# Kernel tuning notes

Hardware: AMD Instinct MI355X
Metric: run time of the kernel (lower is better)

## Reference

```python
import jax, jax.numpy as jnp
import numpy as np

IMG = 512.0          # input H = W
SCORE_THR = 0.05
IOU_THR = 0.5
K_PRE = 1000         # pre-NMS candidates per image
MAX_DET = 300
CLS_OFF = 10000.0    # class-offset trick => per-class NMS


def _make_anchors():
    strides = [8, 16, 32, 64]
    sizes = [32.0, 64.0, 128.0, 256.0]
    ars = [0.5, 1.0, 2.0]
    out = []
    for s, sz in zip(strides, sizes):
        f = int(512 // s)
        ys, xs = np.meshgrid(np.arange(f), np.arange(f), indexing='ij')
        cx = (xs.reshape(-1) + 0.5) * s
        cy = (ys.reshape(-1) + 0.5) * s
        for ar in ars:
            w = sz * np.sqrt(ar)
            h = sz / np.sqrt(ar)
            out.append(np.stack([cx - w / 2, cy - h / 2, cx + w / 2, cy + h / 2], axis=1))
    return np.concatenate(out, axis=0).astype(np.float32)  # (16320, 4)


def setup_inputs() -> dict:
    key = jax.random.key(0)
    k1, k2 = jax.random.split(key)
    anchors = jnp.asarray(_make_anchors())
    B, C = 16, 80
    A = anchors.shape[0]
    cls_preds = jax.random.normal(k1, (B, A, C), jnp.float32) - 2.0  # logits, sigmoid ~0.12
    box_preds = jax.random.normal(k2, (B, A, 4), jnp.float32) * 0.2  # box deltas
    return {"cls_preds": cls_preds, "box_preds": box_preds, "anchors": anchors}


def _decode(anchors, deltas):
    aw = anchors[:, 2] - anchors[:, 0]
    ah = anchors[:, 3] - anchors[:, 1]
    acx = anchors[:, 0] + 0.5 * aw
    acy = anchors[:, 1] + 0.5 * ah
    cx = deltas[:, 0] * aw + acx
    cy = deltas[:, 1] * ah + acy
    w = jnp.exp(deltas[:, 2]) * aw
    h = jnp.exp(deltas[:, 3]) * ah
    b = jnp.stack([cx - 0.5 * w, cy - 0.5 * h, cx + 0.5 * w, cy + 0.5 * h], axis=1)
    return jnp.clip(b, 0.0, IMG)  # clamp to image, H == W == IMG


def _iou_matrix(b):
    area = jnp.maximum(b[:, 2] - b[:, 0], 0.0) * jnp.maximum(b[:, 3] - b[:, 1], 0.0)
    lt = jnp.maximum(b[:, None, :2], b[None, :, :2])
    rb = jnp.minimum(b[:, None, 2:], b[None, :, 2:])
    wh = jnp.clip(rb - lt, 0.0)
    inter = wh[..., 0] * wh[..., 1]
    return inter / jnp.maximum(area[:, None] + area[None, :] - inter, 1e-6)


def _per_image(cls_p, box_p, anchors):
    scores = jax.nn.sigmoid(cls_p)                 # (A, C)
    boxes = _decode(anchors, box_p)                # (A, 4)
    ms = scores.max(axis=1)                        # best class score
    lb = jnp.argmax(scores, axis=1)                # best class id (0-indexed)
    s = jnp.where(ms > SCORE_THR, ms, -1.0)        # score-threshold filter
    top_s, idx = jax.lax.top_k(s, K_PRE)           # pre-NMS candidates, sorted desc
    b = boxes[idx]
    l = lb[idx]
    ob = b + l[:, None].astype(b.dtype) * CLS_OFF  # per-class NMS via offset
    iou = _iou_matrix(ob)                          # (K_PRE, K_PRE)
    rng = jnp.arange(K_PRE)

    def body(i, keep):
        sup = (iou[i] > IOU_THR) & keep[i] & (rng > i)
        return keep & ~sup

    keep = jax.lax.fori_loop(0, K_PRE, body, top_s > 0.0)  # greedy NMS
    fs_all = jnp.where(keep, top_s, -1.0)
    fs, fi = jax.lax.top_k(fs_all, MAX_DET)
    ok = fs > 0.0
    out_boxes = jnp.where(ok[:, None], b[fi], 0.0)
    out_scores = jnp.where(ok, fs, 0.0)
    out_labels = jnp.where(ok, l[fi] + 1, 0)  # labels are 1-indexed
    return out_boxes, out_scores, out_labels


def reference(cls_preds, box_preds, anchors):
    return jax.vmap(lambda c, bp: _per_image(c, bp, anchors))(cls_preds, box_preds)
```

## Files before the change

kernel.cpp:

```cpp
#include <hip/hip_runtime.h>
#include <cstdint>
#include <cmath>

#define NB 16
#define AANCH 16320
#define NCLS 80
#define KPRE 1000
#define MAXDET 300
#define NCH 16
#define CANDCAP 16384
#define HBINS 8192

#define THR_LOGIT -2.9444389791664403f

__global__ __launch_bounds__(256) void k_score(const float* __restrict__ cls,
                                               uint32_t* __restrict__ key,
                                               int* __restrict__ label) {
    int b = blockIdx.y;
    int a0 = blockIdx.x * 64;
    int t = threadIdx.x;
    int al = t >> 2, g = t & 3;
    const float4* p = (const float4*)(cls + ((size_t)b * AANCH + a0) * NCLS) + al * 20 + g;
    float best = -3e38f; int bi = 0;
#pragma unroll
    for (int i = 0; i < 5; ++i) {
        float4 v = p[4 * i];
        int c0 = 4 * g + 16 * i;
        if (v.x > best) { best = v.x; bi = c0 + 0; }
        if (v.y > best) { best = v.y; bi = c0 + 1; }
        if (v.z > best) { best = v.z; bi = c0 + 2; }
        if (v.w > best) { best = v.w; bi = c0 + 3; }
    }
#pragma unroll
    for (int m = 1; m <= 2; m <<= 1) {
        float ob = __shfl_xor(best, m, 64);
        int oi = __shfl_xor(bi, m, 64);
        if (ob > best || (ob == best && oi < bi)) { best = ob; bi = oi; }
    }
    if (g == 0) {
        uint32_t k = 0;
        if (best > THR_LOGIT) {
            uint32_t ub = __float_as_uint(best);
            k = (ub & 0x80000000u) ? ~ub : (ub | 0x80000000u);
        }
        int ag = a0 + al;
        key[(size_t)b * AANCH + ag] = k;
        label[(size_t)b * AANCH + ag] = bi;
    }
}

__global__ __launch_bounds__(1024) void k_fsel(const uint32_t* __restrict__ key,
                                               uint32_t* __restrict__ validCount,
                                               uint32_t* __restrict__ candCount,
                                               uint32_t* __restrict__ candKey,
                                               uint32_t* __restrict__ candIdx) {
    __shared__ uint32_t kk[AANCH];
    __shared__ uint32_t hist[HBINS];
    __shared__ uint32_t part[256];
    __shared__ uint32_t s_pivot, s_pos;
    int b = blockIdx.x, tid = threadIdx.x;
    for (int i = tid; i < HBINS; i += 1024) hist[i] = 0;
    if (tid == 0) s_pos = 0;
    __syncthreads();
    const uint32_t* kb = key + (size_t)b * AANCH;
    for (int i = tid; i < AANCH; i += 1024) {
        uint32_t k = kb[i];
        kk[i] = k;
        atomicAdd(&hist[k >> 19], 1u);
    }
    __syncthreads();
    if (tid < 256) {
        uint32_t s = 0;
#pragma unroll
        for (int i = 0; i < 32; ++i) s += hist[tid * 32 + ((i + tid) & 31)];
        part[tid] = s;
    }
    __syncthreads();
    if (tid == 0) {
        uint32_t acc = 0; int tc = 0;
        for (int t2 = 255; t2 >= 0; --t2) {
            if (acc + part[t2] >= (uint32_t)KPRE) { tc = t2; break; }
            acc += part[t2];
        }
        uint32_t p1 = 0;
        for (int bin = tc * 32 + 31; bin >= tc * 32; --bin) {
            if (acc + hist[bin] >= (uint32_t)KPRE) { p1 = (uint32_t)bin; break; }
            acc += hist[bin];
        }
        s_pivot = p1;
        uint32_t nvalid = (uint32_t)AANCH - hist[0];
        validCount[b] = nvalid < (uint32_t)KPRE ? nvalid : (uint32_t)KPRE;
    }
    __syncthreads();
    uint32_t piv = s_pivot;
    for (int i = tid; i < AANCH; i += 1024) {
        uint32_t k = kk[i];
        if ((k >> 19) >= piv) {
            uint32_t pos = atomicAdd(&s_pos, 1u);
            if (pos < CANDCAP) {
                candKey[(size_t)b * CANDCAP + pos] = k;
                candIdx[(size_t)b * CANDCAP + pos] = (uint32_t)i;
            }
        }
    }
    __syncthreads();
    if (tid == 0) candCount[b] = s_pos < CANDCAP ? s_pos : CANDCAP;
}

__global__ __launch_bounds__(256) void k_rankdec(const uint32_t* __restrict__ candKey,
                                                 const uint32_t* __restrict__ candIdx,
                                                 const uint32_t* __restrict__ candCount,
                                                 const int* __restrict__ label,
                                                 const float* __restrict__ boxp,
                                                 const float* __restrict__ anchors,
                                                 float4* __restrict__ topBox,
                                                 float* __restrict__ topScore,
                                                 int* __restrict__ topLabel) {
    __shared__ unsigned long long tp[2048];
    int b = blockIdx.y, tid = threadIdx.x;
    int C = (int)candCount[b];
    if (blockIdx.x * 256 >= C) return;
    const uint32_t* ck = candKey + (size_t)b * CANDCAP;
    const uint32_t* ci = candIdx + (size_t)b * CANDCAP;
    int c = blockIdx.x * 256 + tid;
    bool h = c < C;
    uint32_t mk = 0, mi = 0;
    if (h) { mk = ck[c]; mi = ci[c]; }
    unsigned long long mine = ((unsigned long long)mk << 32) | (uint32_t)(~mi);
    uint32_t r = 0;
    for (int t0 = 0; t0 < C; t0 += 2048) {
        int n = C - t0; if (n > 2048) n = 2048;
        __syncthreads();
        for (int j = tid; j < n; j += 256)
            tp[j] = ((unsigned long long)ck[t0 + j] << 32) | (uint32_t)(~ci[t0 + j]);
        __syncthreads();
#pragma unroll 4
        for (int j = 0; j < n; ++j) r += (tp[j] > mine);
    }
    if (!h || r >= (uint32_t)KPRE) return;
    uint32_t idx = mi;
    const float* an = anchors + (size_t)idx * 4;
    float a0 = an[0], a1 = an[1], a2 = an[2], a3 = an[3];
    const float* dp = boxp + ((size_t)b * AANCH + idx) * 4;
    float d0 = dp[0], d1 = dp[1], d2 = dp[2], d3 = dp[3];
    float aw = a2 - a0, ah = a3 - a1;
    float acx = a0 + 0.5f * aw, acy = a1 + 0.5f * ah;
    float cx = d0 * aw + acx, cy = d1 * ah + acy;
    float w = expf(d2) * aw, hh = expf(d3) * ah;
    float x1 = fminf(fmaxf(cx - 0.5f * w, 0.0f), 512.0f);
    float y1 = fminf(fmaxf(cy - 0.5f * hh, 0.0f), 512.0f);
    float x2 = fminf(fmaxf(cx + 0.5f * w, 0.0f), 512.0f);
    float y2 = fminf(fmaxf(cy + 0.5f * hh, 0.0f), 512.0f);
    float score;
    if (mk == 0u) {
        score = -1.0f;
    } else {
        uint32_t ub = (mk & 0x80000000u) ? (mk ^ 0x80000000u) : ~mk;
        score = 1.0f / (1.0f + expf(-__uint_as_float(ub)));
    }
    int t = b * KPRE + (int)r;
    topBox[t] = make_float4(x1, y1, x2, y2);
    topScore[t] = score;
    topLabel[t] = label[(size_t)b * AANCH + idx];
}

__global__ __launch_bounds__(64) void k_maskT(const float4* __restrict__ topBox,
                                              const int* __restrict__ topLabel,
                                              unsigned long long* __restrict__ maskT) {
    int b = blockIdx.y;
    int tt = blockIdx.x;
    int rb = 0;
    while (tt >= NCH - rb) { tt -= NCH - rb; ++rb; }
    int cb = rb + tt;
    __shared__ float4 cob[64];
    __shared__ float car[64];
    int lane = threadIdx.x;
    int j = cb * 64 + lane;
    float4 vj;
    if (j < KPRE) {
        vj = topBox[b * KPRE + j];
        float off = (float)topLabel[b * KPRE + j] * 10000.0f;
        vj.x += off; vj.y += off; vj.z += off; vj.w += off;
    } else {
        vj = make_float4(-3e37f, -3e37f, -3e37f, -3e37f);
    }
    cob[lane] = vj;
    car[lane] = fmaxf(vj.z - vj.x, 0.0f) * fmaxf(vj.w - vj.y, 0.0f);
    int i = rb * 64 + lane;
    float4 bi;
    if (i < KPRE) {
        bi = topBox[b * KPRE + i];
        float off = (float)topLabel[b * KPRE + i] * 10000.0f;
        bi.x += off; bi.y += off; bi.z += off; bi.w += off;
    } else {
        bi = make_float4(-3e37f, -3e37f, -3e37f, -3e37f);
    }
    float ai = fmaxf(bi.z - bi.x, 0.0f) * fmaxf(bi.w - bi.y, 0.0f);
    __syncthreads();
    unsigned long long myword = 0;
#pragma unroll 8
    for (int jj = 0; jj < 64; ++jj) {
        int jg = cb * 64 + jj;
        float4 bj = cob[jj];
        float ltx = fmaxf(bi.x, bj.x), lty = fmaxf(bi.y, bj.y);
        float rbx = fminf(bi.z, bj.z), rby = fminf(bi.w, bj.w);
        float wx = fmaxf(rbx - ltx, 0.0f), wy = fmaxf(rby - lty, 0.0f);
        float inter = wx * wy;
        float iou = inter / fmaxf(ai + car[jj] - inter, 1e-6f);
        bool pred = (iou > 0.5f) && (i < jg) && (i < KPRE) && (jg < KPRE);
        unsigned long long bal = __ballot(pred);
        if (lane == jj) myword = bal;
    }
    maskT[(((size_t)b * NCH + rb) * NCH + cb) * 64 + lane] = myword;
}

__global__ __launch_bounds__(64) void k_nmsout(const unsigned long long* __restrict__ maskT,
                                               const uint32_t* __restrict__ validCount,
                                               const float4* __restrict__ topBox,
                                               const float* __restrict__ topScore,
                                               const int* __restrict__ topLabel,
                                               float* __restrict__ out) {
    __shared__ unsigned long long km[NCH];
    __shared__ int pf[NCH + 1];
    int b = blockIdx.x, lane = threadIdx.x;
    int V = (int)validCount[b];
    if (lane < NCH) km[lane] = 0ull;
    __syncthreads();
    const unsigned long long* mtb = maskT + (size_t)b * NCH * NCH * 64;
    int count = 0;
    unsigned long long mt[NCH];
#pragma unroll
    for (int s = 0; s < NCH; ++s) mt[s] = mtb[((size_t)s * NCH + 0) * 64 + lane];
    for (int c = 0; c < NCH; ++c) {
        if (c * 64 >= V || count >= MAXDET) break;
        unsigned long long cur[NCH];
#pragma unroll
        for (int s = 0; s < NCH; ++s) cur[s] = mt[s];
        if (c + 1 < NCH) {
#pragma unroll
            for (int s = 0; s < NCH; ++s) mt[s] = mtb[((size_t)s * NCH + (c + 1)) * 64 + lane];
        }
        unsigned long long dd = 0;
        unsigned long long colbits = 0;
#pragma unroll
        for (int s = 0; s < NCH; ++s) {
            if (s == c) colbits = cur[s];
            dd |= (cur[s] & km[s]);
        }
        bool dead = dd != 0ull;
        bool valid = (c * 64 + lane) < V;
        bool kept = false;
        unsigned long long kmask = 0;
        while (count < MAXDET) {
            unsigned long long undec = __ballot((!dead) && (!kept) && valid);
            if (undec == 0ull) break;
            int f = __builtin_ctzll(undec);
            kmask |= 1ull << f;
            ++count;
            if (lane == f) kept = true;
            dead = dead || (((colbits >> f) & 1ull) != 0ull);
        }
        if (lane == 0) km[c] = kmask;
        __syncthreads();
    }
    __syncthreads();
    if (lane == 0) {
        int acc = 0;
        for (int cc = 0; cc < NCH; ++cc) { pf[cc] = acc; acc += __popcll(km[cc]); }
        pf[NCH] = acc;
    }
    __syncthreads();
    int total = pf[NCH];
    for (int cc = 0; cc < NCH; ++cc) {
        unsigned long long m = km[cc];
        if ((m >> lane) & 1ull) {
            int slot = pf[cc] + __popcll(m & ((1ull << lane) - 1ull));
            int g = cc * 64 + lane;
            int tdx = b * MAXDET + slot;
            float4 box = topBox[b * KPRE + g];
            out[(size_t)tdx * 4 + 0] = box.x;
            out[(size_t)tdx * 4 + 1] = box.y;
            out[(size_t)tdx * 4 + 2] = box.z;
            out[(size_t)tdx * 4 + 3] = box.w;
            out[(size_t)NB * MAXDET * 4 + tdx] = topScore[b * KPRE + g];
            out[(size_t)NB * MAXDET * 5 + tdx] = (float)(topLabel[b * KPRE + g] + 1);
        }
    }
    for (int k = lane; k < MAXDET; k += 64) {
        if (k >= total) {
            int tdx = b * MAXDET + k;
            out[(size_t)tdx * 4 + 0] = 0.0f;
            out[(size_t)tdx * 4 + 1] = 0.0f;
            out[(size_t)tdx * 4 + 2] = 0.0f;
            out[(size_t)tdx * 4 + 3] = 0.0f;
            out[(size_t)NB * MAXDET * 4 + tdx] = 0.0f;
            out[(size_t)NB * MAXDET * 5 + tdx] = 0.0f;
        }
    }
}

extern "C" void kernel_launch(void* const* d_in, const int* in_sizes, int n_in,
                              void* d_out, int out_size, void* d_ws, size_t ws_size,
                              hipStream_t stream) {
    const float* cls = (const float*)d_in[0];
    const float* boxp = (const float*)d_in[1];
    const float* anchors = (const float*)d_in[2];
    float* out = (float*)d_out;

    char* wsp = (char*)d_ws;
    size_t off = 0;
    auto carve = [&](size_t bytes) -> void* {
        void* p = wsp + off;
        off += (bytes + 255) & ~(size_t)255;
        return p;
    };
    unsigned long long* maskT = (unsigned long long*)carve((size_t)NB * NCH * NCH * 64 * 8);
    uint32_t* key       = (uint32_t*)carve((size_t)NB * AANCH * 4);
    int*      label     = (int*)carve((size_t)NB * AANCH * 4);
    uint32_t* candKey   = (uint32_t*)carve((size_t)NB * CANDCAP * 4);
    uint32_t* candIdx   = (uint32_t*)carve((size_t)NB * CANDCAP * 4);
    float4*   topBox    = (float4*)carve((size_t)NB * KPRE * 16);
    float*    topScore  = (float*)carve((size_t)NB * KPRE * 4);
    int*      topLabel  = (int*)carve((size_t)NB * KPRE * 4);
    uint32_t* validCnt  = (uint32_t*)carve((size_t)NB * 4);
    uint32_t* candCount = (uint32_t*)carve((size_t)NB * 4);
    (void)ws_size; (void)out_size; (void)n_in; (void)in_sizes;

    k_score<<<dim3(AANCH / 64, NB), 256, 0, stream>>>(cls, key, label);
    k_fsel<<<NB, 1024, 0, stream>>>(key, validCnt, candCount, candKey, candIdx);
    k_rankdec<<<dim3(CANDCAP / 256, NB), 256, 0, stream>>>(candKey, candIdx, candCount, label,
                                                           boxp, anchors, topBox, topScore,
                                                           topLabel);
    k_maskT<<<dim3(136, NB), 64, 0, stream>>>(topBox, topLabel, maskT);
    k_nmsout<<<NB, 64, 0, stream>>>(maskT, validCnt, topBox, topScore, topLabel, out);
}
```

Before: 217.1 us.

## Fuse all pipeline stages into one cooperative persistent kernel with grid syncs

```diff
diff --git a/kernel.cpp b/kernel.cpp
--- a/kernel.cpp
+++ b/kernel.cpp
@@ -1,6 +1,9 @@
 #include <hip/hip_runtime.h>
+#include <hip/hip_cooperative_groups.h>
 #include <cstdint>
 #include <cmath>
+
+namespace cg = cooperative_groups;
 
 #define NB 16
 #define AANCH 16320
@@ -8,293 +11,284 @@
 #define KPRE 1000
 #define MAXDET 300
 #define NCH 16
-#define CANDCAP 16384
+#define CCAP 4096
 #define HBINS 8192
+#define GRID 256
+#define BLK 1024
 
 #define THR_LOGIT -2.9444389791664403f
 
-__global__ __launch_bounds__(256) void k_score(const float* __restrict__ cls,
-                                               uint32_t* __restrict__ key,
-                                               int* __restrict__ label) {
-    int b = blockIdx.y;
-    int a0 = blockIdx.x * 64;
-    int t = threadIdx.x;
-    int al = t >> 2, g = t & 3;
-    const float4* p = (const float4*)(cls + ((size_t)b * AANCH + a0) * NCLS) + al * 20 + g;
-    float best = -3e38f; int bi = 0;
-#pragma unroll
-    for (int i = 0; i < 5; ++i) {
-        float4 v = p[4 * i];
-        int c0 = 4 * g + 16 * i;
-        if (v.x > best) { best = v.x; bi = c0 + 0; }
-        if (v.y > best) { best = v.y; bi = c0 + 1; }
-        if (v.z > best) { best = v.z; bi = c0 + 2; }
-        if (v.w > best) { best = v.w; bi = c0 + 3; }
-    }
-#pragma unroll
-    for (int m = 1; m <= 2; m <<= 1) {
-        float ob = __shfl_xor(best, m, 64);
-        int oi = __shfl_xor(bi, m, 64);
-        if (ob > best || (ob == best && oi < bi)) { best = ob; bi = oi; }
-    }
-    if (g == 0) {
-        uint32_t k = 0;
-        if (best > THR_LOGIT) {
-            uint32_t ub = __float_as_uint(best);
-            k = (ub & 0x80000000u) ? ~ub : (ub | 0x80000000u);
-        }
-        int ag = a0 + al;
-        key[(size_t)b * AANCH + ag] = k;
-        label[(size_t)b * AANCH + ag] = bi;
-    }
-}
-
-__global__ __launch_bounds__(1024) void k_fsel(const uint32_t* __restrict__ key,
-                                               uint32_t* __restrict__ validCount,
-                                               uint32_t* __restrict__ candCount,
-                                               uint32_t* __restrict__ candKey,
-                                               uint32_t* __restrict__ candIdx) {
-    __shared__ uint32_t kk[AANCH];
+__global__ __launch_bounds__(BLK, 1) void mega(
+    const float* __restrict__ cls, const float* __restrict__ boxp,
+    const float* __restrict__ anchors, float* __restrict__ out,
+    uint32_t* __restrict__ key, int* __restrict__ label,
+    uint32_t* __restrict__ candKey, uint32_t* __restrict__ candIdx,
+    uint32_t* __restrict__ candCount, uint32_t* __restrict__ validCnt,
+    float4* __restrict__ topBox, float* __restrict__ topScore,
+    int* __restrict__ topLabel, unsigned long long* __restrict__ maskT) {
+    cg::grid_group gg = cg::this_grid();
     __shared__ uint32_t hist[HBINS];
+    __shared__ unsigned long long tp[CCAP];
+    __shared__ float4 cobS[16][64];
+    __shared__ float  carS[16][64];
     __shared__ uint32_t part[256];
     __shared__ uint32_t s_pivot, s_pos;
-    int b = blockIdx.x, tid = threadIdx.x;
-    for (int i = tid; i < HBINS; i += 1024) hist[i] = 0;
-    if (tid == 0) s_pos = 0;
-    __syncthreads();
-    const uint32_t* kb = key + (size_t)b * AANCH;
-    for (int i = tid; i < AANCH; i += 1024) {
-        uint32_t k = kb[i];
-        kk[i] = k;
-        atomicAdd(&hist[k >> 19], 1u);
-    }
-    __syncthreads();
-    if (tid < 256) {
-        uint32_t s = 0;
-#pragma unroll
-        for (int i = 0; i < 32; ++i) s += hist[tid * 32 + ((i + tid) & 31)];
-        part[tid] = s;
-    }
-    __syncthreads();
-    if (tid == 0) {
-        uint32_t acc = 0; int tc = 0;
-        for (int t2 = 255; t2 >= 0; --t2) {
-            if (acc + part[t2] >= (uint32_t)KPRE) { tc = t2; break; }
-            acc += part[t2];
-        }
-        uint32_t p1 = 0;
-        for (int bin = tc * 32 + 31; bin >= tc * 32; --bin) {
-            if (acc + hist[bin] >= (uint32_t)KPRE) { p1 = (uint32_t)bin; break; }
-            acc += hist[bin];
-        }
-        s_pivot = p1;
-        uint32_t nvalid = (uint32_t)AANCH - hist[0];
-        validCount[b] = nvalid < (uint32_t)KPRE ? nvalid : (uint32_t)KPRE;
-    }
-    __syncthreads();
-    uint32_t piv = s_pivot;
-    for (int i = tid; i < AANCH; i += 1024) {
-        uint32_t k = kk[i];
-        if ((k >> 19) >= piv) {
-            uint32_t pos = atomicAdd(&s_pos, 1u);
-            if (pos < CANDCAP) {
-                candKey[(size_t)b * CANDCAP + pos] = k;
-                candIdx[(size_t)b * CANDCAP + pos] = (uint32_t)i;
-            }
-        }
-    }
-    __syncthreads();
-    if (tid == 0) candCount[b] = s_pos < CANDCAP ? s_pos : CANDCAP;
-}
-
-__global__ __launch_bounds__(256) void k_rankdec(const uint32_t* __restrict__ candKey,
-                                                 const uint32_t* __restrict__ candIdx,
-                                                 const uint32_t* __restrict__ candCount,
-                                                 const int* __restrict__ label,
-                                                 const float* __restrict__ boxp,
-                                                 const float* __restrict__ anchors,
-                                                 float4* __restrict__ topBox,
-                                                 float* __restrict__ topScore,
-                                                 int* __restrict__ topLabel) {
-    __shared__ unsigned long long tp[2048];
-    int b = blockIdx.y, tid = threadIdx.x;
-    int C = (int)candCount[b];
-    if (blockIdx.x * 256 >= C) return;
-    const uint32_t* ck = candKey + (size_t)b * CANDCAP;
-    const uint32_t* ci = candIdx + (size_t)b * CANDCAP;
-    int c = blockIdx.x * 256 + tid;
-    bool h = c < C;
-    uint32_t mk = 0, mi = 0;
-    if (h) { mk = ck[c]; mi = ci[c]; }
-    unsigned long long mine = ((unsigned long long)mk << 32) | (uint32_t)(~mi);
-    uint32_t r = 0;
-    for (int t0 = 0; t0 < C; t0 += 2048) {
-        int n = C - t0; if (n > 2048) n = 2048;
-        __syncthreads();
-        for (int j = tid; j < n; j += 256)
-            tp[j] = ((unsigned long long)ck[t0 + j] << 32) | (uint32_t)(~ci[t0 + j]);
-        __syncthreads();
+    int tid = threadIdx.x;
+    int bx = blockIdx.x;
+
+    {
+        int T = bx * BLK + tid;
+#pragma unroll
+        for (int it = 0; it < 4; ++it) {
+            int idx4 = it * (GRID * BLK) + T;
+            int am = idx4 >> 2, g = idx4 & 3;
+            bool act = am < NB * AANCH;
+            float best = -3e38f; int bi = 0;
+            if (act) {
+                const float4* p = (const float4*)(cls + (size_t)am * NCLS) + g;
+#pragma unroll
+                for (int i = 0; i < 5; ++i) {
+                    float4 v = p[4 * i];
+                    int c0 = 4 * g + 16 * i;
+                    if (v.x > best) { best = v.x; bi = c0 + 0; }
+                    if (v.y > best) { best = v.y; bi = c0 + 1; }
+                    if (v.z > best) { best = v.z; bi = c0 + 2; }
+                    if (v.w > best) { best = v.w; bi = c0 + 3; }
+                }
+            }
+#pragma unroll
+            for (int m = 1; m <= 2; m <<= 1) {
+                float ob = __shfl_xor(best, m, 64);
+                int oi = __shfl_xor(bi, m, 64);
+                if (ob > best || (ob == best && oi < bi)) { best = ob; bi = oi; }
+            }
+            if (act && g == 0) {
+                uint32_t k = 0;
+                if (best > THR_LOGIT) {
+                    uint32_t ub = __float_as_uint(best);
+                    k = (ub & 0x80000000u) ? ~ub : (ub | 0x80000000u);
+                }
+                key[am] = k;
+                label[am] = bi;
+            }
+        }
+    }
+    gg.sync();
+
+    if (bx < NB) {
+        int b = bx;
+        for (int i = tid; i < HBINS; i += BLK) hist[i] = 0;
+        if (tid == 0) s_pos = 0;
+        __syncthreads();
+        const uint32_t* kb = key + (size_t)b * AANCH;
+        for (int i = tid; i < AANCH; i += BLK) atomicAdd(&hist[kb[i] >> 19], 1u);
+        __syncthreads();
+        if (tid < 256) {
+            uint32_t s = 0;
+#pragma unroll
+            for (int i = 0; i < 32; ++i) s += hist[tid * 32 + ((i + tid) & 31)];
+            part[tid] = s;
+        }
+        __syncthreads();
+        if (tid == 0) {
+            uint32_t acc = 0; int tc = 0;
+            for (int t2 = 255; t2 >= 0; --t2) {
+                if (acc + part[t2] >= (uint32_t)KPRE) { tc = t2; break; }
+                acc += part[t2];
+            }
+            uint32_t p1 = 0;
+            for (int bin = tc * 32 + 31; bin >= tc * 32; --bin) {
+                if (acc + hist[bin] >= (uint32_t)KPRE) { p1 = (uint32_t)bin; break; }
+                acc += hist[bin];
+            }
+            s_pivot = p1;
+            uint32_t nvalid = (uint32_t)AANCH - hist[0];
+            validCnt[b] = nvalid < (uint32_t)KPRE ? nvalid : (uint32_t)KPRE;
+        }
+        __syncthreads();
+        uint32_t piv = s_pivot;
+        for (int i = tid; i < AANCH; i += BLK) {
+            uint32_t k = kb[i];
+            if ((k >> 19) >= piv) {
+                uint32_t pos = atomicAdd(&s_pos, 1u);
+                if (pos < CCAP) {
+                    candKey[(size_t)b * CCAP + pos] = k;
+                    candIdx[(size_t)b * CCAP + pos] = (uint32_t)i;
+                }
+            }
+        }
+        __syncthreads();
+        if (tid == 0) candCount[b] = s_pos < CCAP ? s_pos : CCAP;
+    }
+    gg.sync();
+
+    {
+        int b = bx >> 4, seg = bx & 15;
+        int C = (int)candCount[b];
+        const uint32_t* ck = candKey + (size_t)b * CCAP;
+        const uint32_t* ci = candIdx + (size_t)b * CCAP;
+        for (int j = tid; j < C; j += BLK)
+            tp[j] = ((unsigned long long)ck[j] << 32) | (uint32_t)(~ci[j]);
+        __syncthreads();
+        int c = seg * BLK + tid;
+        if (c < C) {
+            unsigned long long mine = tp[c];
+            uint32_t mk = (uint32_t)(mine >> 32);
+            uint32_t mi = ~(uint32_t)mine;
+            uint32_t r = 0;
 #pragma unroll 4
-        for (int j = 0; j < n; ++j) r += (tp[j] > mine);
-    }
-    if (!h || r >= (uint32_t)KPRE) return;
-    uint32_t idx = mi;
-    const float* an = anchors + (size_t)idx * 4;
-    float a0 = an[0], a1 = an[1], a2 = an[2], a3 = an[3];
-    const float* dp = boxp + ((size_t)b * AANCH + idx) * 4;
-    float d0 = dp[0], d1 = dp[1], d2 = dp[2], d3 = dp[3];
-    float aw = a2 - a0, ah = a3 - a1;
-    float acx = a0 + 0.5f * aw, acy = a1 + 0.5f * ah;
-    float cx = d0 * aw + acx, cy = d1 * ah + acy;
-    float w = expf(d2) * aw, hh = expf(d3) * ah;
-    float x1 = fminf(fmaxf(cx - 0.5f * w, 0.0f), 512.0f);
-    float y1 = fminf(fmaxf(cy - 0.5f * hh, 0.0f), 512.0f);
-    float x2 = fminf(fmaxf(cx + 0.5f * w, 0.0f), 512.0f);
-    float y2 = fminf(fmaxf(cy + 0.5f * hh, 0.0f), 512.0f);
-    float score;
-    if (mk == 0u) {
-        score = -1.0f;
-    } else {
-        uint32_t ub = (mk & 0x80000000u) ? (mk ^ 0x80000000u) : ~mk;
-        score = 1.0f / (1.0f + expf(-__uint_as_float(ub)));
-    }
-    int t = b * KPRE + (int)r;
-    topBox[t] = make_float4(x1, y1, x2, y2);
-    topScore[t] = score;
-    topLabel[t] = label[(size_t)b * AANCH + idx];
-}
-
-__global__ __launch_bounds__(64) void k_maskT(const float4* __restrict__ topBox,
-                                              const int* __restrict__ topLabel,
-                                              unsigned long long* __restrict__ maskT) {
-    int b = blockIdx.y;
-    int tt = blockIdx.x;
-    int rb = 0;
-    while (tt >= NCH - rb) { tt -= NCH - rb; ++rb; }
-    int cb = rb + tt;
-    __shared__ float4 cob[64];
-    __shared__ float car[64];
-    int lane = threadIdx.x;
-    int j = cb * 64 + lane;
-    float4 vj;
-    if (j < KPRE) {
-        vj = topBox[b * KPRE + j];
-        float off = (float)topLabel[b * KPRE + j] * 10000.0f;
-        vj.x += off; vj.y += off; vj.z += off; vj.w += off;
-    } else {
-        vj = make_float4(-3e37f, -3e37f, -3e37f, -3e37f);
-    }
-    cob[lane] = vj;
-    car[lane] = fmaxf(vj.z - vj.x, 0.0f) * fmaxf(vj.w - vj.y, 0.0f);
-    int i = rb * 64 + lane;
-    float4 bi;
-    if (i < KPRE) {
-        bi = topBox[b * KPRE + i];
-        float off = (float)topLabel[b * KPRE + i] * 10000.0f;
-        bi.x += off; bi.y += off; bi.z += off; bi.w += off;
-    } else {
-        bi = make_float4(-3e37f, -3e37f, -3e37f, -3e37f);
-    }
-    float ai = fmaxf(bi.z - bi.x, 0.0f) * fmaxf(bi.w - bi.y, 0.0f);
-    __syncthreads();
-    unsigned long long myword = 0;
+            for (int j = 0; j < C; ++j) r += (tp[j] > mine);
+            if (r < (uint32_t)KPRE) {
+                uint32_t idx = mi;
+                const float* an = anchors + (size_t)idx * 4;
+                float a0 = an[0], a1 = an[1], a2 = an[2], a3 = an[3];
+                const float* dp = boxp + ((size_t)b * AANCH + idx) * 4;
+                float d0 = dp[0], d1 = dp[1], d2 = dp[2], d3 = dp[3];
+                float aw = a2 - a0, ah = a3 - a1;
+                float acx = a0 + 0.5f * aw, acy = a1 + 0.5f * ah;
+                float cx = d0 * aw + acx, cy = d1 * ah + acy;
+                float w = expf(d2) * aw, hh = expf(d3) * ah;
+                float x1 = fminf(fmaxf(cx - 0.5f * w, 0.0f), 512.0f);
+                float y1 = fminf(fmaxf(cy - 0.5f * hh, 0.0f), 512.0f);
+                float x2 = fminf(fmaxf(cx + 0.5f * w, 0.0f), 512.0f);
+                float y2 = fminf(fmaxf(cy + 0.5f * hh, 0.0f), 512.0f);
+                float score;
+                if (mk == 0u) {
+                    score = -1.0f;
+                } else {
+                    uint32_t ub = (mk & 0x80000000u) ? (mk ^ 0x80000000u) : ~mk;
+                    score = 1.0f / (1.0f + expf(-__uint_as_float(ub)));
+                }
+                int t = b * KPRE + (int)r;
+                topBox[t] = make_float4(x1, y1, x2, y2);
+                topScore[t] = score;
+                topLabel[t] = label[(size_t)b * AANCH + idx];
+            }
+        }
+    }
+    gg.sync();
+
+    if (bx < 136) {
+        int w = tid >> 6, lane = tid & 63;
+        int wv = (bx << 4) | w;
+        int b = wv / 136;
+        int tt = wv - b * 136;
+        int rb = 0;
+        while (tt >= NCH - rb) { tt -= NCH - rb; ++rb; }
+        int cb = rb + tt;
+        int j = cb * 64 + lane;
+        float4 vj;
+        if (j < KPRE) {
+            vj = topBox[b * KPRE + j];
+            float off = (float)topLabel[b * KPRE + j] * 10000.0f;
+            vj.x += off; vj.y += off; vj.z += off; vj.w += off;
+        } else {
+            vj = make_float4(-3e37f, -3e37f, -3e37f, -3e37f);
+        }
+        cobS[w][lane] = vj;
+        carS[w][lane] = fmaxf(vj.z - vj.x, 0.0f) * fmaxf(vj.w - vj.y, 0.0f);
+        int i2 = rb * 64 + lane;
+        float4 bi2;
+        if (i2 < KPRE) {
+            bi2 = topBox[b * KPRE + i2];
+            float off = (float)topLabel[b * KPRE + i2] * 10000.0f;
+            bi2.x += off; bi2.y += off; bi2.z += off; bi2.w += off;
+        } else {
+            bi2 = make_float4(-3e37f, -3e37f, -3e37f, -3e37f);
+        }
+        float ai = fmaxf(bi2.z - bi2.x, 0.0f) * fmaxf(bi2.w - bi2.y, 0.0f);
+        __syncthreads();
+        unsigned long long myword = 0;
 #pragma unroll 8
-    for (int jj = 0; jj < 64; ++jj) {
-        int jg = cb * 64 + jj;
-        float4 bj = cob[jj];
-        float ltx = fmaxf(bi.x, bj.x), lty = fmaxf(bi.y, bj.y);
-        float rbx = fminf(bi.z, bj.z), rby = fminf(bi.w, bj.w);
-        float wx = fmaxf(rbx - ltx, 0.0f), wy = fmaxf(rby - lty, 0.0f);
-        float inter = wx * wy;
-        float iou = inter / fmaxf(ai + car[jj] - inter, 1e-6f);
-        bool pred = (iou > 0.5f) && (i < jg) && (i < KPRE) && (jg < KPRE);
-        unsigned long long bal = __ballot(pred);
-        if (lane == jj) myword = bal;
-    }
-    maskT[(((size_t)b * NCH + rb) * NCH + cb) * 64 + lane] = myword;
-}
-
-__global__ __launch_bounds__(64) void k_nmsout(const unsigned long long* __restrict__ maskT,
-                                               const uint32_t* __restrict__ validCount,
-                                               const float4* __restrict__ topBox,
-                                               const float* __restrict__ topScore,
-                                               const int* __restrict__ topLabel,
-                                               float* __restrict__ out) {
-    __shared__ unsigned long long km[NCH];
-    __shared__ int pf[NCH + 1];
-    int b = blockIdx.x, lane = threadIdx.x;
-    int V = (int)validCount[b];
-    if (lane < NCH) km[lane] = 0ull;
-    __syncthreads();
-    const unsigned long long* mtb = maskT + (size_t)b * NCH * NCH * 64;
-    int count = 0;
-    unsigned long long mt[NCH];
-#pragma unroll
-    for (int s = 0; s < NCH; ++s) mt[s] = mtb[((size_t)s * NCH + 0) * 64 + lane];
-    for (int c = 0; c < NCH; ++c) {
-        if (c * 64 >= V || count >= MAXDET) break;
-        unsigned long long cur[NCH];
-#pragma unroll
-        for (int s = 0; s < NCH; ++s) cur[s] = mt[s];
-        if (c + 1 < NCH) {
-#pragma unroll
-            for (int s = 0; s < NCH; ++s) mt[s] = mtb[((size_t)s * NCH + (c + 1)) * 64 + lane];
-        }
-        unsigned long long dd = 0;
-        unsigned long long colbits = 0;
-#pragma unroll
-        for (int s = 0; s < NCH; ++s) {
-            if (s == c) colbits = cur[s];
-            dd |= (cur[s] & km[s]);
-        }
-        bool dead = dd != 0ull;
-        bool valid = (c * 64 + lane) < V;
-        bool kept = false;
-        unsigned long long kmask = 0;
-        while (count < MAXDET) {
-            unsigned long long undec = __ballot((!dead) && (!kept) && valid);
-            if (undec == 0ull) break;
-            int f = __builtin_ctzll(undec);
-            kmask |= 1ull << f;
-            ++count;
-            if (lane == f) kept = true;
-            dead = dead || (((colbits >> f) & 1ull) != 0ull);
-        }
-        if (lane == 0) km[c] = kmask;
-        __syncthreads();
-    }
-    __syncthreads();
-    if (lane == 0) {
-        int acc = 0;
-        for (int cc = 0; cc < NCH; ++cc) { pf[cc] = acc; acc += __popcll(km[cc]); }
-        pf[NCH] = acc;
-    }
-    __syncthreads();
-    int total = pf[NCH];
-    for (int cc = 0; cc < NCH; ++cc) {
-        unsigned long long m = km[cc];
-        if ((m >> lane) & 1ull) {
-            int slot = pf[cc] + __popcll(m & ((1ull << lane) - 1ull));
-            int g = cc * 64 + lane;
-            int tdx = b * MAXDET + slot;
-            float4 box = topBox[b * KPRE + g];
-            out[(size_t)tdx * 4 + 0] = box.x;
-            out[(size_t)tdx * 4 + 1] = box.y;
-            out[(size_t)tdx * 4 + 2] = box.z;
-            out[(size_t)tdx * 4 + 3] = box.w;
-            out[(size_t)NB * MAXDET * 4 + tdx] = topScore[b * KPRE + g];
-            out[(size_t)NB * MAXDET * 5 + tdx] = (float)(topLabel[b * KPRE + g] + 1);
-        }
-    }
-    for (int k = lane; k < MAXDET; k += 64) {
-        if (k >= total) {
-            int tdx = b * MAXDET + k;
-            out[(size_t)tdx * 4 + 0] = 0.0f;
-            out[(size_t)tdx * 4 + 1] = 0.0f;
-            out[(size_t)tdx * 4 + 2] = 0.0f;
-            out[(size_t)tdx * 4 + 3] = 0.0f;
-            out[(size_t)NB * MAXDET * 4 + tdx] = 0.0f;
-            out[(size_t)NB * MAXDET * 5 + tdx] = 0.0f;
+        for (int jj = 0; jj < 64; ++jj) {
+            int jg = cb * 64 + jj;
+            float4 bj = cobS[w][jj];
+            float ltx = fmaxf(bi2.x, bj.x), lty = fmaxf(bi2.y, bj.y);
+            float rbx = fminf(bi2.z, bj.z), rby = fminf(bi2.w, bj.w);
+            float wx = fmaxf(rbx - ltx, 0.0f), wy = fmaxf(rby - lty, 0.0f);
+            float inter = wx * wy;
+            float iou = inter / fmaxf(ai + carS[w][jj] - inter, 1e-6f);
+            bool pred = (iou > 0.5f) && (i2 < jg) && (i2 < KPRE) && (jg < KPRE);
+            unsigned long long bal = __ballot(pred);
+            if (lane == jj) myword = bal;
+        }
+        maskT[(((size_t)b * NCH + rb) * NCH + cb) * 64 + lane] = myword;
+    }
+    gg.sync();
+
+    if (bx < NB && tid < 64) {
+        int b = bx, lane = tid;
+        int V = (int)validCnt[b];
+        const unsigned long long* mtb = maskT + (size_t)b * NCH * NCH * 64;
+        unsigned long long km[NCH];
+#pragma unroll
+        for (int s = 0; s < NCH; ++s) km[s] = 0ull;
+        int count = 0;
+        unsigned long long mt[NCH];
+#pragma unroll
+        for (int s = 0; s < NCH; ++s) mt[s] = mtb[((size_t)s * NCH + 0) * 64 + lane];
+#pragma unroll
+        for (int c = 0; c < NCH; ++c) {
+            bool go = (c * 64 < V) && (count < MAXDET);
+            unsigned long long cur[NCH];
+#pragma unroll
+            for (int s = 0; s < NCH; ++s) cur[s] = mt[s];
+            if (go && c + 1 < NCH) {
+#pragma unroll
+                for (int s = 0; s < NCH; ++s) mt[s] = mtb[((size_t)s * NCH + (c + 1)) * 64 + lane];
+            }
+            unsigned long long kmask = 0;
+            if (go) {
+                unsigned long long dd = 0;
+                unsigned long long colbits = cur[c];
+#pragma unroll
+                for (int s = 0; s < NCH; ++s) dd |= (cur[s] & km[s]);
+                bool dead = dd != 0ull;
+                bool valid = (c * 64 + lane) < V;
+                bool kept = false;
+                while (count < MAXDET) {
+                    unsigned long long undec = __ballot((!dead) && (!kept) && valid);
+                    if (undec == 0ull) break;
+                    int f = __builtin_ctzll(undec);
+                    kmask |= 1ull << f;
+                    ++count;
+                    if (lane == f) kept = true;
+                    dead = dead || (((colbits >> f) & 1ull) != 0ull);
+                }
+            }
+            km[c] = kmask;
+        }
+        int pf[NCH + 1];
+        pf[0] = 0;
+#pragma unroll
+        for (int cc = 0; cc < NCH; ++cc) pf[cc + 1] = pf[cc] + __popcll(km[cc]);
+        int total = pf[NCH];
+#pragma unroll
+        for (int cc = 0; cc < NCH; ++cc) {
+            unsigned long long m = km[cc];
+            if ((m >> lane) & 1ull) {
+                int slot = pf[cc] + __popcll(m & ((1ull << lane) - 1ull));
+                int g = cc * 64 + lane;
+                int tdx = b * MAXDET + slot;
+                float4 box = topBox[b * KPRE + g];
+                out[(size_t)tdx * 4 + 0] = box.x;
+                out[(size_t)tdx * 4 + 1] = box.y;
+                out[(size_t)tdx * 4 + 2] = box.z;
+                out[(size_t)tdx * 4 + 3] = box.w;
+                out[(size_t)NB * MAXDET * 4 + tdx] = topScore[b * KPRE + g];
+                out[(size_t)NB * MAXDET * 5 + tdx] = (float)(topLabel[b * KPRE + g] + 1);
+            }
+        }
+        for (int k2 = lane; k2 < MAXDET; k2 += 64) {
+            if (k2 >= total) {
+                int tdx = b * MAXDET + k2;
+                out[(size_t)tdx * 4 + 0] = 0.0f;
+                out[(size_t)tdx * 4 + 1] = 0.0f;
+                out[(size_t)tdx * 4 + 2] = 0.0f;
+                out[(size_t)tdx * 4 + 3] = 0.0f;
+                out[(size_t)NB * MAXDET * 4 + tdx] = 0.0f;
+                out[(size_t)NB * MAXDET * 5 + tdx] = 0.0f;
+            }
         }
     }
 }
@@ -317,8 +311,8 @@
     unsigned long long* maskT = (unsigned long long*)carve((size_t)NB * NCH * NCH * 64 * 8);
     uint32_t* key       = (uint32_t*)carve((size_t)NB * AANCH * 4);
     int*      label     = (int*)carve((size_t)NB * AANCH * 4);
-    uint32_t* candKey   = (uint32_t*)carve((size_t)NB * CANDCAP * 4);
-    uint32_t* candIdx   = (uint32_t*)carve((size_t)NB * CANDCAP * 4);
+    uint32_t* candKey   = (uint32_t*)carve((size_t)NB * CCAP * 4);
+    uint32_t* candIdx   = (uint32_t*)carve((size_t)NB * CCAP * 4);
     float4*   topBox    = (float4*)carve((size_t)NB * KPRE * 16);
     float*    topScore  = (float*)carve((size_t)NB * KPRE * 4);
     int*      topLabel  = (int*)carve((size_t)NB * KPRE * 4);
@@ -326,11 +320,11 @@
     uint32_t* candCount = (uint32_t*)carve((size_t)NB * 4);
     (void)ws_size; (void)out_size; (void)n_in; (void)in_sizes;
 
-    k_score<<<dim3(AANCH / 64, NB), 256, 0, stream>>>(cls, key, label);
-    k_fsel<<<NB, 1024, 0, stream>>>(key, validCnt, candCount, candKey, candIdx);
-    k_rankdec<<<dim3(CANDCAP / 256, NB), 256, 0, stream>>>(candKey, candIdx, candCount, label,
-                                                           boxp, anchors, topBox, topScore,
-                                                           topLabel);
-    k_maskT<<<dim3(136, NB), 64, 0, stream>>>(topBox, topLabel, maskT);
-    k_nmsout<<<NB, 64, 0, stream>>>(maskT, validCnt, topBox, topScore, topLabel, out);
+    void* args[] = {
+        (void*)&cls, (void*)&boxp, (void*)&anchors, (void*)&out,
+        (void*)&key, (void*)&label, (void*)&candKey, (void*)&candIdx,
+        (void*)&candCount, (void*)&validCnt, (void*)&topBox, (void*)&topScore,
+        (void*)&topLabel, (void*)&maskT
+    };
+    hipLaunchCooperativeKernel((void*)mega, dim3(GRID), dim3(BLK), args, 0, stream);
 }
```

After: 309.2 us. 42.4% more time.
